# Optimization experiments

Measured on AMD Instinct MI355X. Metric: run time of the kernel, lower is better.

## Reference

```python
import jax, jax.numpy as jnp
import numpy as np

N = 50000      # num nodes
E = 800000     # num edges (avg degree 16)
IN, H, OUT = 128, 128, 16
R = 8          # num relations


def rgcn_conv(x, edge_index, edge_type, W, root, bias, num_relations):
    """PyG RGCNConv with aggr='mean': out = x@root + bias + sum_r mean_{j in N_r(i)} x_j @ W_r.
    Mean is linear, so aggregate raw x_j per relation first, then one matmul per relation."""
    src, dst = edge_index[0], edge_index[1]  # messages flow src -> dst
    x_src = x[src]                            # [E, F] gather
    out = x @ root + bias                     # root/self term
    for r in range(num_relations):            # small fixed loop over relations
        m = (edge_type == r).astype(x.dtype)  # [E]
        s = jax.ops.segment_sum(x_src * m[:, None], dst, num_segments=x.shape[0])  # [N, F]
        c = jax.ops.segment_sum(m, dst, num_segments=x.shape[0])                   # [N]
        out = out + (s / jnp.maximum(c, 1.0)[:, None]) @ W[r]
    return out


def setup_inputs() -> dict:
    key = jax.random.key(0)
    ks = jax.random.split(key, 12)
    glorot = lambda k, shape: jax.random.normal(k, shape, jnp.float32) * (2.0 / (shape[-2] + shape[-1])) ** 0.5
    return {
        "x": jax.random.normal(ks[0], (N, IN), jnp.float32),
        "edge_index": jax.random.randint(ks[1], (2, E), 0, N, jnp.int64) if jax.config.read('jax_enable_x64') else jax.random.randint(ks[1], (2, E), 0, N).astype(jnp.int32),
        "edge_type": jax.random.randint(ks[2], (E,), 0, R).astype(jnp.int32),
        "w0": glorot(ks[3], (R, IN, H)),
        "root0": glorot(ks[4], (IN, H)),
        "b0": jnp.zeros((H,), jnp.float32),
        "w1": glorot(ks[5], (R, H, H)),
        "root1": glorot(ks[6], (H, H)),
        "b1": jnp.zeros((H,), jnp.float32),
        "w2": glorot(ks[7], (R, H, OUT)),
        "root2": glorot(ks[8], (H, OUT)),
        "b2": jnp.zeros((OUT,), jnp.float32),
    }


def reference(x, edge_index, edge_type, w0, root0, b0, w1, root1, b1, w2, root2, b2):
    # layer 0: in -> hidden, relu (dropout is identity in eval mode)
    h = jax.nn.relu(rgcn_conv(x, edge_index, edge_type, w0, root0, b0, R))
    # layer 1: hidden -> hidden, relu
    h = jax.nn.relu(rgcn_conv(h, edge_index, edge_type, w1, root1, b1, R))
    # layer 2: hidden -> out (no activation)
    return rgcn_conv(h, edge_index, edge_type, w2, root2, b2, R)
```

## Files before the change

kernel.cpp:

```cpp
#include <hip/hip_runtime.h>

#define N_NODES 50000
#define N_EDGES 800000
#define NREL 8
#define NB8 (N_NODES * NREL)
#define SCAN_T 12500
#define KSTEPS 36
#define A_STRIDE 1160
#define NT32 1563

typedef __attribute__((ext_vector_type(8))) short short8;
typedef __attribute__((ext_vector_type(4))) float f32x4;
typedef __attribute__((ext_vector_type(2))) float f32x2;

__device__ __forceinline__ unsigned short f2bf(float v) {
    union { float f; unsigned int u; } c; c.f = v;
    return (unsigned short)((c.u + 0x7FFFu + ((c.u >> 16) & 1u)) >> 16);
}
__device__ __forceinline__ float bfhi2f(unsigned int u) {
    union { unsigned int u; float f; } c; c.u = u & 0xFFFF0000u; return c.f;
}
__device__ __forceinline__ float bflo2f(unsigned int u) {
    union { unsigned int u; float f; } c; c.u = u << 16; return c.f;
}

#define PREP_Z   (NB8 / 4)
#define PREP_X   (N_NODES * 32)
#define PREP_P   (8 * KSTEPS * 64)
#define PREP_P2  (1 * KSTEPS * 64)
#define PREP_TOTAL (PREP_Z + PREP_X + 2 * PREP_P + PREP_P2)

__device__ __forceinline__ void pack_one(int idx, const float* __restrict__ root,
                                         const float* __restrict__ W,
                                         unsigned short* __restrict__ Wpack, int FOUT) {
    int lane = idx & 63;
    int ks = (idx >> 6) % KSTEPS;
    int ct = idx / (KSTEPS * 64);
    int kbase = ks * 32 + (lane >> 4) * 8;
    int col = ct * 16 + (lane & 15);
    union { unsigned short us[8]; uint4 v; } u;
#pragma unroll
    for (int j = 0; j < 8; j++) {
        int k = kbase + j;
        float val = (k < 128) ? root[(size_t)k * FOUT + col]
                              : W[(size_t)(k - 128) * FOUT + col];
        u.us[j] = f2bf(val);
    }
    ((uint4*)Wpack)[idx] = u.v;
}

__global__ void prep_kernel(const float* __restrict__ X, unsigned int* __restrict__ Xb2,
                            const float* __restrict__ r0, const float* __restrict__ w0,
                            unsigned short* __restrict__ Wp0,
                            const float* __restrict__ r1, const float* __restrict__ w1,
                            unsigned short* __restrict__ Wp1,
                            const float* __restrict__ r2, const float* __restrict__ w2,
                            unsigned short* __restrict__ Wp2,
                            int* __restrict__ cnt) {
    int t = blockIdx.x * blockDim.x + threadIdx.x;
    if (t < PREP_Z) { ((int4*)cnt)[t] = make_int4(0, 0, 0, 0); return; }
    t -= PREP_Z;
    if (t < PREP_X) {
        float4 v = ((const float4*)X)[t];
        unsigned int p0 = (unsigned int)f2bf(v.x) | ((unsigned int)f2bf(v.y) << 16);
        unsigned int p1 = (unsigned int)f2bf(v.z) | ((unsigned int)f2bf(v.w) << 16);
        ((uint2*)Xb2)[t] = make_uint2(p0, p1);
        return;
    }
    t -= PREP_X;
    if (t < PREP_P) { pack_one(t, r0, w0, Wp0, 128); return; }
    t -= PREP_P;
    if (t < PREP_P) { pack_one(t, r1, w1, Wp1, 128); return; }
    t -= PREP_P;
    if (t < PREP_P2) pack_one(t, r2, w2, Wp2, 16);
}

__global__ void count_kernel(const int* __restrict__ ei, const int* __restrict__ et,
                             int* __restrict__ cnt, int E) {
    int e = blockIdx.x * blockDim.x + threadIdx.x;
    if (e >= E) return;
    int d = ei[E + e];
    int t = et[e];
    atomicAdd(&cnt[d * NREL + t], 1);
}

__global__ void scanA_kernel(const int* __restrict__ cnt, int* __restrict__ tsum) {
    int g = blockIdx.x * blockDim.x + threadIdx.x;
    if (g >= SCAN_T) return;
    const int4* p = (const int4*)(cnt + (size_t)g * 32);
    int s = 0;
#pragma unroll
    for (int j = 0; j < 8; j++) {
        int4 v = p[j];
        s += v.x + v.y + v.z + v.w;
    }
    tsum[g] = s;
}

__global__ void scanB_kernel(const int* __restrict__ tsum, int* __restrict__ toff) {
    __shared__ int part[1024];
    int t = threadIdx.x;
    const int C = 13;
    int n0 = t * C, n1 = n0 + C; if (n1 > SCAN_T) n1 = SCAN_T;
    int s = 0;
    for (int n = n0; n < n1; n++) s += tsum[n];
    part[t] = s;
    __syncthreads();
    for (int off = 1; off < 1024; off <<= 1) {
        int v = (t >= off) ? part[t - off] : 0;
        __syncthreads();
        part[t] += v;
        __syncthreads();
    }
    int run = (t > 0) ? part[t - 1] : 0;
    for (int n = n0; n < n1; n++) { toff[n] = run; run += tsum[n]; }
}

__global__ void scanC_kernel(const int* __restrict__ cnt, const int* __restrict__ toff,
                             int* __restrict__ rs8, int* __restrict__ live) {
    int b = blockIdx.x * blockDim.x + threadIdx.x;
    if (b >= NB8) return;
    int c = cnt[b];
    int s = c;
#pragma unroll
    for (int d = 1; d < 32; d <<= 1) {
        int v = __shfl_up(s, d, 32);
        if ((threadIdx.x & 31) >= d) s += v;
    }
    int val = toff[b >> 5] + (s - c);
    rs8[b] = val;
    live[b] = val;
    if (b == 0) rs8[NB8] = N_EDGES;
}

__global__ void place_kernel(const int* __restrict__ ei, const int* __restrict__ et,
                             int* __restrict__ live,
                             unsigned short* __restrict__ csr_src, int E) {
    int e = blockIdx.x * blockDim.x + threadIdx.x;
    if (e >= E) return;
    int s = ei[e];
    int d = ei[E + e];
    int t = et[e];
    int pos = atomicAdd(&live[d * NREL + t], 1);
    csr_src[pos] = (unsigned short)s;
}

template <int FOUT, bool RELU>
__global__ __launch_bounds__(1024, 8) void layer_kernel(
    const unsigned int* __restrict__ Xb2,
    const int* __restrict__ rs8,
    const unsigned short* __restrict__ csr_src,
    const unsigned short* __restrict__ Wpack,
    const float* __restrict__ bias,
    void* __restrict__ Yout)
{
    __shared__ __align__(16) unsigned short Abuf[32][A_STRIDE];

    int tid = threadIdx.x;
    int wave = tid >> 6, lane = tid & 63;
    int l15 = lane & 15;
    int node0 = blockIdx.x * 32;

    int gn0 = node0 + wave * 2;
    if (gn0 < N_NODES) {
        unsigned int* row0 = (unsigned int*)&Abuf[wave * 2][0];
        unsigned int* row1 = (unsigned int*)&Abuf[wave * 2 + 1][0];

        int bl = lane <= 16 ? lane : 16;
        int bv = rs8[gn0 * 8 + bl];
        unsigned int self0 = Xb2[(size_t)gn0 * 64 + lane];
        unsigned int self1 = Xb2[(size_t)(gn0 + 1) * 64 + lane];

        int e     = __builtin_amdgcn_readlane(bv, 0);
        int e_end = __builtin_amdgcn_readlane(bv, 16);

        row0[lane] = self0;
        row1[lane] = self1;

        int r = 0;
        int segs = e;
        int be = __builtin_amdgcn_readlane(bv, 1);
        f32x2 av = (f32x2){0.f, 0.f};

#define FLUSH_R()                                                              \
        do {                                                                   \
            int c_ = be - segs;                                                \
            float iv_ = __builtin_amdgcn_rcpf((float)(c_ > 0 ? c_ : 1));       \
            unsigned int pk_;                                                  \
            asm("v_cvt_pk_bf16_f32 %0, %1, %2"                                 \
                : "=v"(pk_) : "v"(av.x * iv_), "v"(av.y * iv_));               \
            unsigned int* rw_ = (r < 8) ? row0 : row1;                         \
            rw_[(1 + (r & 7)) * 64 + lane] = pk_;                              \
            av = (f32x2){0.f, 0.f}; segs = be; r++;                            \
            be = __builtin_amdgcn_readlane(bv, r + 1 <= 16 ? r + 1 : 16);      \
        } while (0)

        if (e < e_end) {
            int e1m = e_end - 1;
            int ma = e + l15; if (ma > e1m) ma = e1m;
            unsigned int mv = csr_src[ma];
            while (e < e_end) {
                int bn = e_end - e; if (bn > 16) bn = 16;
                int sc[16];
#pragma unroll
                for (int k = 0; k < 16; k++) sc[k] = __builtin_amdgcn_readlane((int)mv, k);
                unsigned int xp[16];
#pragma unroll
                for (int k = 0; k < 16; k++) xp[k] = Xb2[(size_t)sc[k] * 64 + lane];
                int en = e + bn;
                if (en < e_end) {
                    int mb = en + l15; if (mb > e1m) mb = e1m;
                    mv = csr_src[mb];
                }
#pragma unroll
                for (int k = 0; k < 16; k++) {
                    if (k < bn) {
                        int ec = e + k;
                        while (ec >= be) FLUSH_R();
                        av += (f32x2){bflo2f(xp[k]), bfhi2f(xp[k])};
                    }
                }
                e = en;
            }
        }
        while (r < 16) FLUSH_R();
#undef FLUSH_R
    }
    __syncthreads();

    int quad = lane >> 4, l16 = lane & 15;
    int swz = lane & 7;
    if constexpr (FOUT == 128) {
        int ct = wave & 7, kh = wave >> 3;
        f32x4 acc0 = (f32x4){0.f, 0.f, 0.f, 0.f};
        f32x4 acc1 = (f32x4){0.f, 0.f, 0.f, 0.f};
        int ks0 = kh * 18;
        for (int ks = ks0; ks < ks0 + 18; ks++) {
            short8 b = *(const short8*)(Wpack + (((size_t)ct * KSTEPS + ks) * 64 + lane) * 8);
            short8 a0 = *(const short8*)&Abuf[l16][ks * 32 + quad * 8];
            short8 a1 = *(const short8*)&Abuf[16 + l16][ks * 32 + quad * 8];
            acc0 = __builtin_amdgcn_mfma_f32_16x16x32_bf16(a0, b, acc0, 0, 0, 0);
            acc1 = __builtin_amdgcn_mfma_f32_16x16x32_bf16(a1, b, acc1, 0, 0, 0);
        }
        __syncthreads();
        f32x4* rv = (f32x4*)&Abuf[0][0];
        if (wave >= 8) {
            int sb = ((wave - 8) * 64 + lane) * 2;
            rv[sb ^ swz]       = acc0;
            rv[(sb + 1) ^ swz] = acc1;
        }
        __syncthreads();
        if (wave < 8) {
            int sb = (wave * 64 + lane) * 2;
            f32x4 s0 = acc0 + rv[sb ^ swz];
            f32x4 s1 = acc1 + rv[(sb + 1) ^ swz];
            unsigned short* Yb = (unsigned short*)Yout;
            int h = ct * 16 + l16;
            float bvs = bias[h];
#pragma unroll
            for (int r4 = 0; r4 < 4; r4++) {
                int n0r = node0 + quad * 4 + r4;
                float v0 = s0[r4] + bvs;
                if (RELU) v0 = v0 > 0.f ? v0 : 0.f;
                Yb[(size_t)n0r * 128 + h] = f2bf(v0);
                int n1r = node0 + 16 + quad * 4 + r4;
                float v1 = s1[r4] + bvs;
                if (RELU) v1 = v1 > 0.f ? v1 : 0.f;
                if (n1r < N_NODES) Yb[(size_t)n1r * 128 + h] = f2bf(v1);
            }
        }
    } else {
        int ks0 = (wave < 4) ? wave * 3 : 12 + (wave - 4) * 2;
        int ksn = (wave < 4) ? 3 : 2;
        f32x4 acc0 = (f32x4){0.f, 0.f, 0.f, 0.f};
        f32x4 acc1 = (f32x4){0.f, 0.f, 0.f, 0.f};
        for (int ks = ks0; ks < ks0 + ksn; ks++) {
            short8 b = *(const short8*)(Wpack + ((size_t)ks * 64 + lane) * 8);
            short8 a0 = *(const short8*)&Abuf[l16][ks * 32 + quad * 8];
            short8 a1 = *(const short8*)&Abuf[16 + l16][ks * 32 + quad * 8];
            acc0 = __builtin_amdgcn_mfma_f32_16x16x32_bf16(a0, b, acc0, 0, 0, 0);
            acc1 = __builtin_amdgcn_mfma_f32_16x16x32_bf16(a1, b, acc1, 0, 0, 0);
        }
        __syncthreads();
        float* red = (float*)&Abuf[0][0];
        f32x4* rv = (f32x4*)red;
        int sb = (wave * 64 + lane) * 2;
        rv[sb ^ swz]       = acc0;
        rv[(sb + 1) ^ swz] = acc1;
        __syncthreads();
        if (tid < 512) {
            int nr = tid >> 4, h = tid & 15;
            int g = nr >> 4, rem = nr & 15;
            int q_ = rem >> 2, r4 = rem & 3;
            int lsrc = q_ * 16 + h;
            float s = 0.f;
#pragma unroll
            for (int w2 = 0; w2 < 16; w2++) {
                int sl = ((w2 * 64 + lsrc) * 2 + g) ^ (lsrc & 7);
                s += red[sl * 4 + r4];
            }
            int node = node0 + nr;
            float v = s + bias[h];
            if (RELU) v = v > 0.f ? v : 0.f;
            if (node < N_NODES)
                ((float*)Yout)[(size_t)node * 16 + h] = v;
        }
    }
}

extern "C" void kernel_launch(void* const* d_in, const int* in_sizes, int n_in,
                              void* d_out, int out_size, void* d_ws, size_t ws_size,
                              hipStream_t stream) {
    const float* x  = (const float*)d_in[0];
    const int*   ei = (const int*)d_in[1];
    const int*   et = (const int*)d_in[2];
    const float* w0 = (const float*)d_in[3];
    const float* r0 = (const float*)d_in[4];
    const float* b0 = (const float*)d_in[5];
    const float* w1 = (const float*)d_in[6];
    const float* r1 = (const float*)d_in[7];
    const float* b1 = (const float*)d_in[8];
    const float* w2 = (const float*)d_in[9];
    const float* r2 = (const float*)d_in[10];
    const float* b2 = (const float*)d_in[11];

    char* wsp = (char*)d_ws;
    size_t off = 0;
    auto alloc = [&](size_t bytes) -> void* {
        void* p = wsp + off;
        off += (bytes + 255) & ~(size_t)255;
        return p;
    };

    int* cnt    = (int*)alloc((size_t)NB8 * 4);
    int* rs8    = (int*)alloc(((size_t)NB8 + 1) * 4);
    int* live   = (int*)alloc((size_t)NB8 * 4);
    int* tsum   = (int*)alloc((size_t)SCAN_T * 4);
    int* toff   = (int*)alloc((size_t)SCAN_T * 4);
    unsigned short* csr_src = (unsigned short*)alloc((size_t)N_EDGES * 2);
    unsigned short* Wp0 = (unsigned short*)alloc((size_t)8 * KSTEPS * 64 * 8 * 2);
    unsigned short* Wp1 = (unsigned short*)alloc((size_t)8 * KSTEPS * 64 * 8 * 2);
    unsigned short* Wp2 = (unsigned short*)alloc((size_t)1 * KSTEPS * 64 * 8 * 2);
    unsigned int* Xb = (unsigned int*)alloc((size_t)N_NODES * 64 * 4);
    unsigned int* H0 = (unsigned int*)alloc((size_t)N_NODES * 64 * 4);
    unsigned int* H1 = (unsigned int*)alloc((size_t)N_NODES * 64 * 4);

    prep_kernel<<<dim3((PREP_TOTAL + 255) / 256), dim3(256), 0, stream>>>(
        x, Xb, r0, w0, Wp0, r1, w1, Wp1, r2, w2, Wp2, cnt);
    count_kernel<<<dim3((N_EDGES + 255) / 256), dim3(256), 0, stream>>>(ei, et, cnt, N_EDGES);
    scanA_kernel<<<dim3((SCAN_T + 255) / 256), dim3(256), 0, stream>>>(cnt, tsum);
    scanB_kernel<<<dim3(1), dim3(1024), 0, stream>>>(tsum, toff);
    scanC_kernel<<<dim3((NB8 + 255) / 256), dim3(256), 0, stream>>>(cnt, toff, rs8, live);
    place_kernel<<<dim3((N_EDGES + 255) / 256), dim3(256), 0, stream>>>(ei, et, live,
                                                                        csr_src, N_EDGES);

    layer_kernel<128, true ><<<dim3(NT32), dim3(1024), 0, stream>>>(
        Xb, rs8, csr_src, Wp0, b0, (void*)H0);
    layer_kernel<128, true ><<<dim3(NT32), dim3(1024), 0, stream>>>(
        H0, rs8, csr_src, Wp1, b1, (void*)H1);
    layer_kernel<16, false><<<dim3(NT32), dim3(1024), 0, stream>>>(
        H1, rs8, csr_src, Wp2, b2, d_out);
}
```

Baseline: 323.8 us.

## Balance edge aggregation across waves by splitting block edges into equal chunks

Each block now loads its 257 segment boundaries into shared memory and divides the block's edge range into 16 equal chunks. Each wave finds its (node, relation) segment range by binary search, so waves no longer own fixed node pairs and are no longer unbalanced by degree variation. This adds a shared-memory load, an extra barrier and binary searches per wave. Segments are still assigned whole to one wave, so per-segment work can still be uneven.

```diff
diff --git a/kernel.cpp b/kernel.cpp
--- a/kernel.cpp
+++ b/kernel.cpp
@@ -155,32 +155,53 @@
     void* __restrict__ Yout)
 {
     __shared__ __align__(16) unsigned short Abuf[32][A_STRIDE];
+    __shared__ int sbnd[257];
 
     int tid = threadIdx.x;
     int wave = tid >> 6, lane = tid & 63;
     int l15 = lane & 15;
     int node0 = blockIdx.x * 32;
 
+    if (tid <= 256) {
+        int idx = node0 * 8 + tid;
+        if (idx > NB8) idx = NB8;
+        sbnd[tid] = rs8[idx];
+    }
     int gn0 = node0 + wave * 2;
-    if (gn0 < N_NODES) {
-        unsigned int* row0 = (unsigned int*)&Abuf[wave * 2][0];
-        unsigned int* row1 = (unsigned int*)&Abuf[wave * 2 + 1][0];
-
-        int bl = lane <= 16 ? lane : 16;
-        int bv = rs8[gn0 * 8 + bl];
-        unsigned int self0 = Xb2[(size_t)gn0 * 64 + lane];
-        unsigned int self1 = Xb2[(size_t)(gn0 + 1) * 64 + lane];
-
-        int e     = __builtin_amdgcn_readlane(bv, 0);
-        int e_end = __builtin_amdgcn_readlane(bv, 16);
-
-        row0[lane] = self0;
-        row1[lane] = self1;
-
-        int r = 0;
-        int segs = e;
-        int be = __builtin_amdgcn_readlane(bv, 1);
+    bool wr_self = (gn0 + 1 < N_NODES);
+    unsigned int self0 = 0, self1 = 0;
+    if (wr_self) {
+        self0 = Xb2[(size_t)gn0 * 64 + lane];
+        self1 = Xb2[(size_t)(gn0 + 1) * 64 + lane];
+    }
+    __syncthreads();
+
+    {
+        if (wr_self) {
+            ((unsigned int*)&Abuf[wave * 2][0])[lane] = self0;
+            ((unsigned int*)&Abuf[wave * 2 + 1][0])[lane] = self1;
+        }
+
+        int e0 = sbnd[0], e1 = sbnd[256];
+        int nE = e1 - e0;
+        int chunk = (nE + 15) >> 4;
+
+        auto lbound = [&](int target) {
+            int lo = 0, hi = 256;
+            while (lo < hi) {
+                int mid = (lo + hi) >> 1;
+                if (sbnd[mid] >= target) hi = mid; else lo = mid + 1;
+            }
+            return lo;
+        };
+        int s     = (wave == 0)  ? 0   : lbound(e0 + wave * chunk);
+        int s_end = (wave == 15) ? 256 : lbound(e0 + (wave + 1) * chunk);
+
+        int segs = sbnd[s];
+        int be   = sbnd[s < 256 ? s + 1 : 256];
         f32x2 av = (f32x2){0.f, 0.f};
+        int e = segs;
+        int wend = sbnd[s_end];
 
 #define FLUSH_R()                                                              \
         do {                                                                   \
@@ -189,18 +210,17 @@
             unsigned int pk_;                                                  \
             asm("v_cvt_pk_bf16_f32 %0, %1, %2"                                 \
                 : "=v"(pk_) : "v"(av.x * iv_), "v"(av.y * iv_));               \
-            unsigned int* rw_ = (r < 8) ? row0 : row1;                         \
-            rw_[(1 + (r & 7)) * 64 + lane] = pk_;                              \
-            av = (f32x2){0.f, 0.f}; segs = be; r++;                            \
-            be = __builtin_amdgcn_readlane(bv, r + 1 <= 16 ? r + 1 : 16);      \
+            ((unsigned int*)&Abuf[s >> 3][0])[(1 + (s & 7)) * 64 + lane] = pk_;\
+            av = (f32x2){0.f, 0.f}; segs = be; s++;                            \
+            be = sbnd[s < 256 ? s + 1 : 256];                                  \
         } while (0)
 
-        if (e < e_end) {
-            int e1m = e_end - 1;
+        if (e < wend) {
+            int e1m = e1 - 1;
             int ma = e + l15; if (ma > e1m) ma = e1m;
             unsigned int mv = csr_src[ma];
-            while (e < e_end) {
-                int bn = e_end - e; if (bn > 16) bn = 16;
+            while (e < wend) {
+                int bn = wend - e; if (bn > 16) bn = 16;
                 int sc[16];
 #pragma unroll
                 for (int k = 0; k < 16; k++) sc[k] = __builtin_amdgcn_readlane((int)mv, k);
@@ -208,7 +228,7 @@
 #pragma unroll
                 for (int k = 0; k < 16; k++) xp[k] = Xb2[(size_t)sc[k] * 64 + lane];
                 int en = e + bn;
-                if (en < e_end) {
+                if (en < wend) {
                     int mb = en + l15; if (mb > e1m) mb = e1m;
                     mv = csr_src[mb];
                 }
@@ -223,7 +243,7 @@
                 e = en;
             }
         }
-        while (r < 16) FLUSH_R();
+        while (s < s_end) FLUSH_R();
 #undef FLUSH_R
     }
     __syncthreads();
```

After: 358.8 us. 10.8% more time.
